# Performance work log

Hardware: AMD Instinct MI355X
Metric: run time of the kernel (lower is better)

The kernel has to match this reference:

```python
import jax, jax.numpy as jnp
import numpy as np

B, NQ, NKV, D, H, HD = 8, 1024, 2048, 1024, 16, 64  # inner_dim = H*HD = 1024


def setup_inputs() -> dict:
    key = jax.random.key(0)
    ks = jax.random.split(key, 10)
    s = 0.02
    return {
        "latent": jax.random.normal(ks[0], (B, NQ, D), jnp.float32),
        "data": jax.random.normal(ks[1], (B, NKV, D), jnp.float32),
        "wq": jax.random.normal(ks[2], (D, H * HD), jnp.float32) * s,
        "bq": jax.random.normal(ks[3], (H * HD,), jnp.float32) * s,
        "wk": jax.random.normal(ks[4], (D, H * HD), jnp.float32) * s,
        "bk": jax.random.normal(ks[5], (H * HD,), jnp.float32) * s,
        "wv": jax.random.normal(ks[6], (D, H * HD), jnp.float32) * s,
        "bv": jax.random.normal(ks[7], (H * HD,), jnp.float32) * s,
        "wo": jax.random.normal(ks[8], (H * HD, D), jnp.float32) * s,
        "bo": jax.random.normal(ks[9], (D,), jnp.float32) * s,
    }


def reference(latent, data, wq, bq, wk, bk, wv, bv, wo, bo):
    scale = HD ** -0.5
    # projections: [b, n, H*HD] -> [b, h, n, d]
    def split_heads(t):
        b, n, _ = t.shape
        return t.reshape(b, n, H, HD).transpose(0, 2, 1, 3)

    q = split_heads(latent @ wq + bq)   # [b, h, nq, d]
    k = split_heads(data @ wk + bk)     # [b, h, nkv, d]
    v = split_heads(data @ wv + bv)     # [b, h, nkv, d]

    scores = jnp.einsum("bhid,bhjd->bhij", q, k) * scale  # [b, h, nq, nkv]
    att = jax.nn.softmax(scores, axis=-1)                  # dropout p=0 (eval)
    out = jnp.einsum("bhij,bhjd->bhid", att, v)            # [b, h, nq, d]
    out = out.transpose(0, 2, 1, 3).reshape(B, NQ, H * HD)
    return out @ wo + bo
```

## Files before the change

### kernel.cpp

```cpp
#include <hip/hip_runtime.h>
#include <hip/hip_bf16.h>
#include <math.h>


using short8  = __attribute__((ext_vector_type(8))) short;
using f32x4   = __attribute__((ext_vector_type(4))) float;
using uint4v  = __attribute__((ext_vector_type(4))) unsigned int;

__device__ __forceinline__ ushort f2bf(float f) {
    unsigned u = __builtin_bit_cast(unsigned, f);
    u = (u + 0x7FFFu + ((u >> 16) & 1u)) >> 16;
    return (ushort)u;
}
__device__ __forceinline__ unsigned pack_bf2(float lo, float hi) {
    unsigned ulo = __builtin_bit_cast(unsigned, lo) + 0x8000u;
    unsigned uhi = __builtin_bit_cast(unsigned, hi) + 0x8000u;
    return __builtin_amdgcn_perm(uhi, ulo, 0x07060302);
}

__device__ __forceinline__ void gld_lds16(const ushort* g, ushort* l) {
    __builtin_amdgcn_global_load_lds(
        (const __attribute__((address_space(1))) unsigned int*)(const void*)g,
        (__attribute__((address_space(3))) unsigned int*)(void*)l,
        16, 0, 0);
}

__global__ void cvt_bf16(const float* __restrict__ in, ushort* __restrict__ out, int n) {
    int i = (blockIdx.x * blockDim.x + threadIdx.x) * 8;
    if (i >= n) return;
    float4 a = *(const float4*)(in + i);
    float4 b = *(const float4*)(in + i + 4);
    short8 o;
    o[0] = (short)f2bf(a.x); o[1] = (short)f2bf(a.y);
    o[2] = (short)f2bf(a.z); o[3] = (short)f2bf(a.w);
    o[4] = (short)f2bf(b.x); o[5] = (short)f2bf(b.y);
    o[6] = (short)f2bf(b.z); o[7] = (short)f2bf(b.w);
    *(short8*)(out + i) = o;
}

__global__ void transpose_w(const float* __restrict__ w0, const float* __restrict__ w1,
                            const float* __restrict__ w2, const float* __restrict__ w3,
                            ushort* __restrict__ o0, ushort* __restrict__ o1,
                            ushort* __restrict__ o2, ushort* __restrict__ o3) {
    __shared__ ushort tile[32][33];
    int z = blockIdx.z;
    const float* in = (z == 0) ? w0 : (z == 1) ? w1 : (z == 2) ? w2 : w3;
    ushort* out     = (z == 0) ? o0 : (z == 1) ? o1 : (z == 2) ? o2 : o3;
    int tx = threadIdx.x, ty = threadIdx.y;
    int x = blockIdx.x * 32 + tx;
    int y = blockIdx.y * 32;
#pragma unroll
    for (int i = 0; i < 32; i += 8)
        tile[ty + i][tx] = f2bf(in[(size_t)(y + ty + i) * 1024 + x]);
    __syncthreads();
    int x2 = blockIdx.y * 32 + tx;
    int y2 = blockIdx.x * 32;
#pragma unroll
    for (int i = 0; i < 32; i += 8)
        out[(size_t)(y2 + ty + i) * 1024 + x2] = tile[tx][ty + i];
}

template <int MODE>
__global__ void gemm_bt(const ushort* __restrict__ A, const ushort* __restrict__ Bt,
                        const float* __restrict__ bias, void* __restrict__ Cv,
                        int K, float scale) {
    __shared__ __align__(16) ushort As[128 * 32];
    __shared__ __align__(16) ushort Bs[128 * 32];
    const int tid  = threadIdx.x;
    const int wave = tid >> 6, lane = tid & 63;
    const int l15 = lane & 15, quad = lane >> 4;
    const int wm = wave & 1, wn = wave >> 1;
    const int m0 = blockIdx.x * 128;
    const int n0 = blockIdx.y * 128;

    f32x4 acc[4][4] = {};

    for (int k0 = 0; k0 < K; k0 += 32) {
        __syncthreads();
#pragma unroll
        for (int i = 0; i < 2; ++i) {
            int f   = (i * 256 + tid) * 8;
            int row = f >> 5, col = f & 31;
            gld_lds16(A  + (size_t)(m0 + row) * K + k0 + col, As + (i * 256 + wave * 64) * 8);
            gld_lds16(Bt + (size_t)(n0 + row) * K + k0 + col, Bs + (i * 256 + wave * 64) * 8);
        }
        __syncthreads();

        short8 a[4], b[4];
#pragma unroll
        for (int mi = 0; mi < 4; ++mi)
            a[mi] = *(const short8*)(As + (wm * 64 + mi * 16 + l15) * 32 + quad * 8);
#pragma unroll
        for (int ni = 0; ni < 4; ++ni)
            b[ni] = *(const short8*)(Bs + (wn * 64 + ni * 16 + l15) * 32 + quad * 8);
#pragma unroll
        for (int mi = 0; mi < 4; ++mi)
#pragma unroll
            for (int ni = 0; ni < 4; ++ni)
                acc[mi][ni] = __builtin_amdgcn_mfma_f32_16x16x32_bf16(a[mi], b[ni], acc[mi][ni], 0, 0, 0);
    }

    float bv[4];
    int   cols[4];
#pragma unroll
    for (int ni = 0; ni < 4; ++ni) {
        cols[ni] = n0 + wn * 64 + ni * 16 + l15;
        bv[ni]   = bias[cols[ni]];
    }
#pragma unroll
    for (int mi = 0; mi < 4; ++mi) {
        int rbase = m0 + wm * 64 + mi * 16 + quad * 4;
#pragma unroll
        for (int ni = 0; ni < 4; ++ni) {
            float v[4];
#pragma unroll
            for (int rr = 0; rr < 4; ++rr)
                v[rr] = (acc[mi][ni][rr] + bv[ni]) * scale;
            if (MODE == 1) {
                int kvl = rbase & 2047;
                int pos = (kvl & ~31) + ((kvl >> 2) & 3) * 8 + ((kvl >> 4) & 1) * 4;
                size_t base = ((size_t)((rbase >> 11) * 1024 + cols[ni])) * 2048 + pos;
                uint2 o;
                o.x = pack_bf2(v[0], v[1]);
                o.y = pack_bf2(v[2], v[3]);
                *(uint2*)((ushort*)Cv + base) = o;
            } else {
#pragma unroll
                for (int rr = 0; rr < 4; ++rr) {
                    int row = rbase + rr;
                    if (MODE == 0)
                        ((ushort*)Cv)[(size_t)row * 1024 + cols[ni]] = f2bf(v[rr]);
                    else
                        ((float*)Cv)[(size_t)row * 1024 + cols[ni]] = v[rr];
                }
            }
        }
    }
}

__global__ __launch_bounds__(256, 4) void attn_fused(const ushort* __restrict__ Q,
                                                     const ushort* __restrict__ K,
                                                     const ushort* __restrict__ Vt,
                                                     ushort* __restrict__ O) {
    __shared__ __align__(16) ushort smem[2 * 8192];
    ushort* Ks  = smem;
    ushort* Vts = smem + 8192;

    const int tid  = threadIdx.x;
    const int wave = tid >> 6, lane = tid & 63;
    const int l15 = lane & 15, quad = lane >> 4;
    const int bx = blockIdx.x;
    const int bh = bx & 127, h = bh & 15, b = bh >> 4;
    const int q0 = (bx >> 7) * 128;

    const ushort* Qg = Q + ((size_t)(b * 1024 + q0)) * 1024 + h * 64;
    const ushort* Kg = K + ((size_t)(b * 2048)) * 1024 + h * 64;
    const ushort* Vg = Vt + ((size_t)(b * 1024 + h * 64)) * 2048;

    short8 bq[2][2];
#pragma unroll
    for (int qt = 0; qt < 2; ++qt) {
        int row = wave * 32 + qt * 16 + l15;
#pragma unroll
        for (int ks = 0; ks < 2; ++ks)
            bq[ks][qt] = *(const short8*)(Qg + (size_t)row * 1024 + ks * 32 + quad * 8);
    }

    f32x4 Oacc[4][2] = {};
    float l_run[2] = {0.f, 0.f};

    const int rig = lane >> 3;
    const int scb8 = (lane & 7) ^ rig;
    const int riv = lane >> 4;
    const int cb16 = lane & 15;

    for (int kv0 = 0; kv0 < 2048; kv0 += 128) {
        __syncthreads();
#pragma unroll
        for (int g = 0; g < 4; ++g) {
            int G = wave * 4 + g;
            gld_lds16(Kg + (size_t)(kv0 + G * 8 + rig) * 1024 + scb8 * 8, Ks + G * 512);
            int vrow = G * 4 + riv;
            int scv = cb16 ^ (vrow & 15);
            gld_lds16(Vg + (size_t)vrow * 2048 + kv0 + scv * 8, Vts + G * 512);
        }
        __syncthreads();

        unsigned pk[8][2][2];
#pragma unroll
        for (int kvt = 0; kvt < 8; ++kvt) {
            f32x4 s0 = {}, s1 = {};
#pragma unroll
            for (int ks = 0; ks < 2; ++ks) {
                int ck = ((ks * 4 + quad) ^ (l15 & 7)) * 8;
                short8 ak = *(const short8*)(Ks + (kvt * 16 + l15) * 64 + ck);
                s0 = __builtin_amdgcn_mfma_f32_16x16x32_bf16(ak, bq[ks][0], s0, 0, 0, 0);
                s1 = __builtin_amdgcn_mfma_f32_16x16x32_bf16(ak, bq[ks][1], s1, 0, 0, 0);
            }
            float p0[4], p1[4];
#pragma unroll
            for (int rr = 0; rr < 4; ++rr) {
                p0[rr] = __builtin_amdgcn_exp2f(s0[rr]);
                p1[rr] = __builtin_amdgcn_exp2f(s1[rr]);
                l_run[0] += p0[rr];
                l_run[1] += p1[rr];
            }
            pk[kvt][0][0] = pack_bf2(p0[0], p0[1]);
            pk[kvt][0][1] = pack_bf2(p0[2], p0[3]);
            pk[kvt][1][0] = pack_bf2(p1[0], p1[1]);
            pk[kvt][1][1] = pack_bf2(p1[2], p1[3]);
        }

#pragma unroll
        for (int sp = 0; sp < 4; ++sp) {
#pragma unroll
            for (int dt = 0; dt < 4; ++dt) {
                int cv = ((sp * 4 + quad) ^ l15) * 8;
                short8 av = *(const short8*)(Vts + (dt * 16 + l15) * 128 + cv);
#pragma unroll
                for (int qt = 0; qt < 2; ++qt) {
                    uint4v u = {pk[2 * sp][qt][0], pk[2 * sp][qt][1],
                                pk[2 * sp + 1][qt][0], pk[2 * sp + 1][qt][1]};
                    short8 bp = __builtin_bit_cast(short8, u);
                    Oacc[dt][qt] = __builtin_amdgcn_mfma_f32_16x16x32_bf16(av, bp, Oacc[dt][qt], 0, 0, 0);
                }
            }
        }
    }

#pragma unroll
    for (int qt = 0; qt < 2; ++qt) {
        float l = l_run[qt];
        l += __shfl_xor(l, 16);
        l += __shfl_xor(l, 32);
        float inv = 1.f / l;
        int qg = q0 + wave * 32 + qt * 16 + l15;
#pragma unroll
        for (int dt = 0; dt < 4; ++dt) {
            uint2 o;
            o.x = pack_bf2(Oacc[dt][qt][0] * inv, Oacc[dt][qt][1] * inv);
            o.y = pack_bf2(Oacc[dt][qt][2] * inv, Oacc[dt][qt][3] * inv);
            *(uint2*)(O + ((size_t)(b * 1024 + qg)) * 1024 + h * 64 + dt * 16 + quad * 4) = o;
        }
    }
}

extern "C" void kernel_launch(void* const* d_in, const int* in_sizes, int n_in,
                              void* d_out, int out_size, void* d_ws, size_t ws_size,
                              hipStream_t stream) {
    const float* latent = (const float*)d_in[0];
    const float* data   = (const float*)d_in[1];
    const float* wq     = (const float*)d_in[2];
    const float* bq     = (const float*)d_in[3];
    const float* wk     = (const float*)d_in[4];
    const float* bk     = (const float*)d_in[5];
    const float* wv     = (const float*)d_in[6];
    const float* bv     = (const float*)d_in[7];
    const float* wo     = (const float*)d_in[8];
    const float* bo     = (const float*)d_in[9];
    float* out = (float*)d_out;

    ushort* ws   = (ushort*)d_ws;
    ushort* wqT  = ws;
    ushort* wkT  = wqT + (1u << 20);
    ushort* wvT  = wkT + (1u << 20);
    ushort* woT  = wvT + (1u << 20);
    ushort* latB = woT + (1u << 20);
    ushort* datB = latB + (8u << 20);
    ushort* Qb   = datB + (16u << 20);
    ushort* Kb   = Qb + (8u << 20);
    ushort* Vtb  = Kb + (16u << 20);
    ushort* AO   = Vtb + (16u << 20);

    cvt_bf16<<<(8u << 20) / (256 * 8), 256, 0, stream>>>(latent, latB, 8u << 20);
    cvt_bf16<<<(16u << 20) / (256 * 8), 256, 0, stream>>>(data, datB, 16u << 20);
    transpose_w<<<dim3(32, 32, 4), dim3(32, 8), 0, stream>>>(wq, wk, wv, wo, wqT, wkT, wvT, woT);

    const float qscale = 0.125f * 1.44269504088896340736f;
    gemm_bt<0><<<dim3(64, 8), 256, 0, stream>>>(latB, wqT, bq, Qb, 1024, qscale);
    gemm_bt<0><<<dim3(128, 8), 256, 0, stream>>>(datB, wkT, bk, Kb, 1024, 1.0f);
    gemm_bt<1><<<dim3(128, 8), 256, 0, stream>>>(datB, wvT, bv, Vtb, 1024, 1.0f);
    attn_fused<<<dim3(1024), 256, 0, stream>>>(Qb, Kb, Vtb, AO);
    gemm_bt<2><<<dim3(64, 8), 256, 0, stream>>>(AO, woT, bo, out, 1024, 1.0f);
}
```

Before: 383.5 us.

## Replace projection GEMMs with pipelined 256x256 tiles and merge QKV launches

Replaces the simple 128x128, single-buffered bf16 GEMM with a 256x256-tile, 512-thread kernel. It double-buffers 64-wide K slices in 128KB of LDS with an XOR swizzle, interleaves async global-to-LDS loads with MFMA phases, and raises wave priority around the MFMAs. The Q, K and V projections are merged into one launch of 640 blocks, and the output projection uses the same body. The aim is more data reuse per block, less LDS bank conflict, overlapped loads, and fewer launches. The cost is the large LDS footprint and hand-placed waitcnt/barrier scheduling, which limit occupancy and are fragile to get right. The output projection also drops to only 128 blocks.

```diff
diff --git a/kernel.cpp b/kernel.cpp
--- a/kernel.cpp
+++ b/kernel.cpp
@@ -60,82 +60,178 @@
         out[(size_t)(y2 + ty + i) * 1024 + x2] = tile[tx][ty + i];
 }
 
-template <int MODE>
-__global__ void gemm_bt(const ushort* __restrict__ A, const ushort* __restrict__ Bt,
-                        const float* __restrict__ bias, void* __restrict__ Cv,
-                        int K, float scale) {
-    __shared__ __align__(16) ushort As[128 * 32];
-    __shared__ __align__(16) ushort Bs[128 * 32];
+template <int S>
+__device__ __forceinline__ void stage_half(const ushort* __restrict__ G, int rbase,
+                                           ushort* tile, int H, int kcol,
+                                           int wave, int lane) {
+#pragma unroll
+    for (int c = 0; c < 2; ++c) {
+        int rho = c * 64 + wave * 8;
+        int gr0 = (rho / S) * (2 * S) + H * S + (rho % S);
+        int rig = lane >> 3;
+        int q   = (lane & 7) ^ rig;
+        gld_lds16(G + (size_t)(rbase + gr0 + rig) * 1024 + kcol + q * 8,
+                  tile + gr0 * 64);
+    }
+}
+
+__device__ __forceinline__ void gemm256_body(
+        const ushort* __restrict__ A, const ushort* __restrict__ Bt,
+        const float* __restrict__ bias, void* __restrict__ Cv,
+        float scale, int mode, int bm, int bn) {
+    __shared__ __align__(16) ushort sm[65536];
+    ushort* As0 = sm;
+    ushort* Bs0 = sm + 16384;
+    ushort* As1 = sm + 32768;
+    ushort* Bs1 = sm + 49152;
+
     const int tid  = threadIdx.x;
     const int wave = tid >> 6, lane = tid & 63;
     const int l15 = lane & 15, quad = lane >> 4;
-    const int wm = wave & 1, wn = wave >> 1;
-    const int m0 = blockIdx.x * 128;
-    const int n0 = blockIdx.y * 128;
-
-    f32x4 acc[4][4] = {};
-
-    for (int k0 = 0; k0 < K; k0 += 32) {
-        __syncthreads();
-#pragma unroll
-        for (int i = 0; i < 2; ++i) {
-            int f   = (i * 256 + tid) * 8;
-            int row = f >> 5, col = f & 31;
-            gld_lds16(A  + (size_t)(m0 + row) * K + k0 + col, As + (i * 256 + wave * 64) * 8);
-            gld_lds16(Bt + (size_t)(n0 + row) * K + k0 + col, Bs + (i * 256 + wave * 64) * 8);
-        }
-        __syncthreads();
-
-        short8 a[4], b[4];
-#pragma unroll
-        for (int mi = 0; mi < 4; ++mi)
-            a[mi] = *(const short8*)(As + (wm * 64 + mi * 16 + l15) * 32 + quad * 8);
-#pragma unroll
-        for (int ni = 0; ni < 4; ++ni)
-            b[ni] = *(const short8*)(Bs + (wn * 64 + ni * 16 + l15) * 32 + quad * 8);
-#pragma unroll
-        for (int mi = 0; mi < 4; ++mi)
-#pragma unroll
-            for (int ni = 0; ni < 4; ++ni)
-                acc[mi][ni] = __builtin_amdgcn_mfma_f32_16x16x32_bf16(a[mi], b[ni], acc[mi][ni], 0, 0, 0);
-    }
-
-    float bv[4];
+    const int wm = wave >> 2, wn = wave & 3;
+    const int m0 = bm * 256, n0 = bn * 256;
+
+    const int rA  = wm * 128 + l15;
+    const int rB  = wn * 64 + l15;
+    const int cq0 = quad ^ (l15 & 7);
+    const int cq1 = (4 + quad) ^ (l15 & 7);
+
+    stage_half<64>(A,  m0, As0, 0, 0,  wave, lane);
+    stage_half<32>(Bt, n0, Bs0, 0, 0,  wave, lane);
+    stage_half<32>(Bt, n0, Bs0, 1, 0,  wave, lane);
+    stage_half<64>(A,  m0, As0, 1, 0,  wave, lane);
+    stage_half<64>(A,  m0, As1, 0, 64, wave, lane);
+    stage_half<32>(Bt, n0, Bs1, 1, 64, wave, lane);
+    stage_half<64>(A,  m0, As1, 1, 64, wave, lane);
+    asm volatile("s_waitcnt vmcnt(6)" ::: "memory");
+    __builtin_amdgcn_s_barrier();
+
+    f32x4 acc[8][4] = {};
+
+#define LDA(MH)                                                                   \
+    _Pragma("unroll")                                                             \
+    for (int mi = 0; mi < 4; ++mi) {                                              \
+        a[mi][0] = *(const short8*)(Ac + (rA + (MH) * 64 + mi * 16) * 64 + cq0 * 8); \
+        a[mi][1] = *(const short8*)(Ac + (rA + (MH) * 64 + mi * 16) * 64 + cq1 * 8); \
+    }
+#define LDB(NH)                                                                   \
+    _Pragma("unroll")                                                             \
+    for (int ni = 0; ni < 2; ++ni) {                                              \
+        b[ni][0] = *(const short8*)(Bc + (rB + (NH) * 32 + ni * 16) * 64 + cq0 * 8); \
+        b[ni][1] = *(const short8*)(Bc + (rB + (NH) * 32 + ni * 16) * 64 + cq1 * 8); \
+    }
+#define MFMA_PHASE(MB, NB)                                                        \
+    __builtin_amdgcn_s_barrier();                                                 \
+    asm volatile("s_waitcnt lgkmcnt(0)" ::: "memory");                            \
+    __builtin_amdgcn_sched_barrier(0);                                            \
+    __builtin_amdgcn_s_setprio(1);                                                \
+    _Pragma("unroll")                                                             \
+    for (int mi = 0; mi < 4; ++mi)                                                \
+        _Pragma("unroll")                                                         \
+        for (int ni = 0; ni < 2; ++ni)                                            \
+            _Pragma("unroll")                                                     \
+            for (int kk = 0; kk < 2; ++kk)                                        \
+                acc[(MB) * 4 + mi][(NB) * 2 + ni] =                               \
+                    __builtin_amdgcn_mfma_f32_16x16x32_bf16(                      \
+                        a[mi][kk], b[ni][kk], acc[(MB) * 4 + mi][(NB) * 2 + ni],  \
+                        0, 0, 0);                                                 \
+    __builtin_amdgcn_s_setprio(0);                                                \
+    __builtin_amdgcn_s_barrier();
+
+#pragma unroll 2
+    for (int g = 0; g < 16; ++g) {
+        ushort* Ac = (g & 1) ? As1 : As0;
+        ushort* Bc = (g & 1) ? Bs1 : Bs0;
+        ushort* Bn = (g & 1) ? Bs0 : Bs1;
+        const int k1 = ((g + 1) & 15) * 64;
+        const int k2 = ((g + 2) & 15) * 64;
+        short8 a[4][2], b[2][2];
+
+        LDA(0) LDB(0)
+        stage_half<32>(Bt, n0, Bn, 0, k1, wave, lane);
+        MFMA_PHASE(0, 0)
+
+        LDB(1)
+        stage_half<64>(A, m0, Ac, 0, k2, wave, lane);
+        MFMA_PHASE(0, 1)
+
+        LDA(1)
+        stage_half<32>(Bt, n0, Bc, 1, k2, wave, lane);
+        MFMA_PHASE(1, 1)
+
+        LDB(0)
+        stage_half<64>(A, m0, Ac, 1, k2, wave, lane);
+        asm volatile("s_waitcnt vmcnt(6)" ::: "memory");
+        MFMA_PHASE(1, 0)
+    }
+#undef LDA
+#undef LDB
+#undef MFMA_PHASE
+
+    asm volatile("s_waitcnt vmcnt(0)" ::: "memory");
+
+    float bvv[4];
     int   cols[4];
 #pragma unroll
-    for (int ni = 0; ni < 4; ++ni) {
-        cols[ni] = n0 + wn * 64 + ni * 16 + l15;
-        bv[ni]   = bias[cols[ni]];
-    }
-#pragma unroll
-    for (int mi = 0; mi < 4; ++mi) {
-        int rbase = m0 + wm * 64 + mi * 16 + quad * 4;
-#pragma unroll
-        for (int ni = 0; ni < 4; ++ni) {
+    for (int n4 = 0; n4 < 4; ++n4) {
+        cols[n4] = n0 + wn * 64 + n4 * 16 + l15;
+        bvv[n4]  = bias[cols[n4]];
+    }
+#pragma unroll
+    for (int m8 = 0; m8 < 8; ++m8) {
+        int rbase = m0 + wm * 128 + m8 * 16 + quad * 4;
+#pragma unroll
+        for (int n4 = 0; n4 < 4; ++n4) {
             float v[4];
 #pragma unroll
             for (int rr = 0; rr < 4; ++rr)
-                v[rr] = (acc[mi][ni][rr] + bv[ni]) * scale;
-            if (MODE == 1) {
+                v[rr] = (acc[m8][n4][rr] + bvv[n4]) * scale;
+            if (mode == 1) {
                 int kvl = rbase & 2047;
                 int pos = (kvl & ~31) + ((kvl >> 2) & 3) * 8 + ((kvl >> 4) & 1) * 4;
-                size_t base = ((size_t)((rbase >> 11) * 1024 + cols[ni])) * 2048 + pos;
+                size_t base = ((size_t)((rbase >> 11) * 1024 + cols[n4])) * 2048 + pos;
                 uint2 o;
                 o.x = pack_bf2(v[0], v[1]);
                 o.y = pack_bf2(v[2], v[3]);
                 *(uint2*)((ushort*)Cv + base) = o;
+            } else if (mode == 0) {
+#pragma unroll
+                for (int rr = 0; rr < 4; ++rr)
+                    ((ushort*)Cv)[(size_t)(rbase + rr) * 1024 + cols[n4]] = f2bf(v[rr]);
             } else {
 #pragma unroll
-                for (int rr = 0; rr < 4; ++rr) {
-                    int row = rbase + rr;
-                    if (MODE == 0)
-                        ((ushort*)Cv)[(size_t)row * 1024 + cols[ni]] = f2bf(v[rr]);
-                    else
-                        ((float*)Cv)[(size_t)row * 1024 + cols[ni]] = v[rr];
-                }
+                for (int rr = 0; rr < 4; ++rr)
+                    ((float*)Cv)[(size_t)(rbase + rr) * 1024 + cols[n4]] = v[rr];
             }
         }
     }
+}
+
+__global__ __launch_bounds__(512, 2) void proj_qkv(
+        const ushort* __restrict__ latB, const ushort* __restrict__ datB,
+        const ushort* __restrict__ wqT, const ushort* __restrict__ wkT,
+        const ushort* __restrict__ wvT,
+        const float* __restrict__ bq, const float* __restrict__ bk,
+        const float* __restrict__ bv,
+        ushort* __restrict__ Qb, ushort* __restrict__ Kb, ushort* __restrict__ Vtb,
+        float qscale) {
+    int bid = blockIdx.x;
+    const ushort* A;
+    const ushort* W;
+    const float*  bias;
+    void*         C;
+    float sc;
+    int mode, idx;
+    if (bid < 128)      { A = latB; W = wqT; bias = bq; C = Qb;  sc = qscale; mode = 0; idx = bid; }
+    else if (bid < 384) { A = datB; W = wkT; bias = bk; C = Kb;  sc = 1.f;    mode = 0; idx = bid - 128; }
+    else                { A = datB; W = wvT; bias = bv; C = Vtb; sc = 1.f;    mode = 1; idx = bid - 384; }
+    gemm256_body(A, W, bias, C, sc, mode, idx >> 2, idx & 3);
+}
+
+__global__ __launch_bounds__(512, 2) void gemm256_o(
+        const ushort* __restrict__ A, const ushort* __restrict__ W,
+        const float* __restrict__ bias, float* __restrict__ C) {
+    gemm256_body(A, W, bias, C, 1.f, 2, (int)blockIdx.x >> 2, (int)blockIdx.x & 3);
 }
 
 __global__ __launch_bounds__(256, 4) void attn_fused(const ushort* __restrict__ Q,
@@ -277,9 +373,8 @@
     transpose_w<<<dim3(32, 32, 4), dim3(32, 8), 0, stream>>>(wq, wk, wv, wo, wqT, wkT, wvT, woT);
 
     const float qscale = 0.125f * 1.44269504088896340736f;
-    gemm_bt<0><<<dim3(64, 8), 256, 0, stream>>>(latB, wqT, bq, Qb, 1024, qscale);
-    gemm_bt<0><<<dim3(128, 8), 256, 0, stream>>>(datB, wkT, bk, Kb, 1024, 1.0f);
-    gemm_bt<1><<<dim3(128, 8), 256, 0, stream>>>(datB, wvT, bv, Vtb, 1024, 1.0f);
+    proj_qkv<<<dim3(640), 512, 0, stream>>>(latB, datB, wqT, wkT, wvT,
+                                            bq, bk, bv, Qb, Kb, Vtb, qscale);
     attn_fused<<<dim3(1024), 256, 0, stream>>>(Qb, Kb, Vtb, AO);
-    gemm_bt<2><<<dim3(64, 8), 256, 0, stream>>>(AO, woT, bo, out, 1024, 1.0f);
-}
+    gemm256_o<<<dim3(128), 512, 0, stream>>>(AO, woT, bo, out);
+}
```

New measurement: 392.5 us. +2.4%, slower.
